# Optimization experiments

Hardware: AMD Instinct MI355X
Metric: run time of the kernel (lower is better)

## Reference

```python
import jax, jax.numpy as jnp
import numpy as np

T_STEPS = 4
LAYERS = 10
CYCLE = 10
C = 64
TAU = 1.2
V_TH = 0.5
SG_ALPHA = 4.0  # spikingjelly default surrogate.Sigmoid alpha


@jax.custom_vjp
def heaviside_sg(x):
    return (x >= 0.0).astype(x.dtype)

def _h_fwd(x):
    return heaviside_sg(x), x

def _h_bwd(x, g):
    s = jax.nn.sigmoid(SG_ALPHA * x)
    return (SG_ALPHA * s * (1.0 - s) * g,)

heaviside_sg.defvjp(_h_fwd, _h_bwd)


def lif(x_seq):
    # MultiStepLIFNode: v' = v + (x - (v - v_reset))/tau, hard reset to v_reset=0,
    # detach_reset=True -> spike in reset path is stop-gradient'ed.
    def step(v, x):
        v = v + (x - v) / TAU
        spike = heaviside_sg(v - V_TH)
        v = v * (1.0 - jax.lax.stop_gradient(spike))
        return v, spike
    _, spikes = jax.lax.scan(step, jnp.zeros_like(x_seq[0]), x_seq)
    return spikes


def conv_seq(x, w, b, dilation=1):
    # x: [T,B,Cin,L]; w: [Cout,Cin,K]; 'same' padding for odd K
    T, B, Ci, L = x.shape
    K = w.shape[-1]
    pad = (K - 1) * dilation // 2
    y = jax.lax.conv_general_dilated(
        x.reshape(T * B, Ci, L), w, (1,), [(pad, pad)],
        rhs_dilation=(dilation,), dimension_numbers=('NCH', 'OIH', 'NCH'))
    y = y + b[None, :, None]
    return y.reshape(T, B, -1, L)


def setup_inputs() -> dict:
    key = jax.random.key(0)
    ks = jax.random.split(key, 20)
    B, L = 4, 4096
    s = 0.1
    n = jax.random.normal
    inp = {
        'audio': jax.random.uniform(ks[0], (B, L), dtype=jnp.float32),
        'diffusion_step': jax.random.randint(ks[1], (B,), 0, 50),
        'W_in': n(ks[2], (C, 1, 1), jnp.float32) * s,
        'b_in': n(ks[3], (C,), jnp.float32) * s,
        'demb_w1': n(ks[4], (LAYERS, C, 1), jnp.float32) * s,
        'demb_b1': n(ks[5], (LAYERS, C), jnp.float32) * s,
        'demb_w2': n(ks[6], (LAYERS, C, C), jnp.float32) * s,
        'demb_b2': n(ks[7], (LAYERS, C), jnp.float32) * s,
        'dproj_w': n(ks[8], (LAYERS, C, C), jnp.float32) * s,
        'dproj_b': n(ks[9], (LAYERS, C), jnp.float32) * s,
        'conv_w': n(ks[10], (LAYERS, 2 * C, C, 3), jnp.float32) * 0.05,
        'conv_b': n(ks[11], (LAYERS, 2 * C), jnp.float32) * s,
        'skip_w': n(ks[12], (LAYERS, C, C, 1), jnp.float32) * s,
        'skip_b': n(ks[13], (LAYERS, C), jnp.float32) * s,
        'res_w': n(ks[14], (LAYERS, C, C, 1), jnp.float32) * s,
        'res_b': n(ks[15], (LAYERS, C), jnp.float32) * s,
        'W_out': n(ks[16], (1, C, 1), jnp.float32) * s,
        'b_out': n(ks[17], (1,), jnp.float32) * s,
    }
    return inp


def reference(audio, diffusion_step, W_in, b_in, demb_w1, demb_b1, demb_w2,
              demb_b2, dproj_w, dproj_b, conv_w, conv_b, skip_w, skip_b,
              res_w, res_b, W_out, b_out):
    B, L = audio.shape
    # Poisson encoder: spike = 1[u < x] per timestep (fixed key -> deterministic)
    u = jax.random.uniform(jax.random.key(42), (T_STEPS, B, 1, L), dtype=jnp.float32)
    spike_seq = (u < audio[None, :, None, :]).astype(jnp.float32)

    x = conv_seq(spike_seq, W_in, b_in)          # [T,B,C,L]
    x = lif(x)

    d = diffusion_step.astype(jnp.float32)[:, None]  # [B,1]
    total_skip = jnp.zeros_like(x)
    for i in range(LAYERS):
        dilation = 2 ** (i % CYCLE)
        emb = jax.nn.silu(d @ demb_w1[i].T + demb_b1[i]) @ demb_w2[i].T + demb_b2[i]  # [B,C]
        proj = emb @ dproj_w[i].T + dproj_b[i]                                        # [B,C]
        y = x + proj[None, :, :, None]
        y = conv_seq(y, conv_w[i], conv_b[i], dilation=dilation)  # [T,B,2C,L]
        y = lif(y)
        gate, filt = jnp.split(y, 2, axis=2)
        y = jax.nn.sigmoid(gate) * jnp.tanh(filt)
        total_skip = total_skip + conv_seq(y, skip_w[i], skip_b[i])
        x = x + conv_seq(y, res_w[i], res_b[i])

    total_skip = jax.nn.relu(total_skip)
    out = conv_seq(total_skip, W_out, b_out)  # [T,B,1,L]
    out = lif(out)
    return out.sum(axis=0)  # [B,1,L]
```

## Files before the change

### kernel.cpp

```cpp
#include <hip/hip_runtime.h>

#define LL 4096
#define NB 4
#define NC 64
#define NT 4
#define NLAYERS 10
#define XS 5120
#define XPAD 512

typedef float v2f __attribute__((ext_vector_type(2)));

typedef __attribute__((address_space(4))) const float cfloat;
__device__ __forceinline__ cfloat* to_constant(const float* p) {
  return (cfloat*)(unsigned long long)p;
}

__device__ __forceinline__ void threefry2x32(unsigned x0, unsigned x1,
                                             unsigned& o0, unsigned& o1) {
  const unsigned ks0 = 0u, ks1 = 42u;
  const unsigned ks2 = 0x1BD11BDAu ^ ks0 ^ ks1;
  const unsigned ks[3] = {ks0, ks1, ks2};
  const unsigned r0[4] = {13u, 15u, 26u, 6u};
  const unsigned r1[4] = {17u, 29u, 16u, 24u};
  x0 += ks0; x1 += ks1;
#pragma unroll
  for (int g = 0; g < 5; ++g) {
    const unsigned* rr = (g & 1) ? r1 : r0;
#pragma unroll
    for (int j = 0; j < 4; ++j) {
      x0 += x1;
      unsigned r = rr[j];
      x1 = (x1 << r) | (x1 >> (32u - r));
      x1 ^= x0;
    }
    x0 += ks[(g + 1) % 3];
    x1 += ks[(g + 2) % 3] + (unsigned)(g + 1);
  }
  o0 = x0; o1 = x1;
}

__device__ __forceinline__ float u01(unsigned bits) {
  return __uint_as_float((bits >> 9) | 0x3f800000u) - 1.0f;
}

__device__ __forceinline__ float lif_step(float& v, float xt) {
  v = v + (xt - v) / 1.2f;
  float s = (v >= 0.5f) ? 1.0f : 0.0f;
  v = v * (1.0f - s);
  return s;
}

__global__ void prep_kernel(const float* __restrict__ skip_w,
                            const float* __restrict__ res_w,
                            const float* __restrict__ conv_w,
                            float* __restrict__ skipT,
                            float* __restrict__ resT,
                            float* __restrict__ wT) {
  int i = blockIdx.x;
  for (int idx = threadIdx.x; idx < 4096; idx += 256) {
    int c = idx >> 6, cp = idx & 63;
    skipT[i * 4096 + cp * 64 + c] = skip_w[i * 4096 + c * 64 + cp];
    resT[i * 4096 + cp * 64 + c] = res_w[i * 4096 + c * 64 + cp];
  }
  for (int idx = threadIdx.x; idx < 16 * 64 * 3 * 8; idx += 256) {
    int col = idx & 7;
    int r = idx >> 3;
    int k = r % 3; r /= 3;
    int ci = r % 64;
    int g = r / 64;
    int co = (col < 4) ? (g * 4 + col) : (64 + g * 4 + (col - 4));
    wT[i * 24576 + idx] = conv_w[(i * 128 + co) * 192 + ci * 3 + k];
  }
}

__global__ void proj_kernel(const int* __restrict__ dstep,
                            const float* __restrict__ w1, const float* __restrict__ b1,
                            const float* __restrict__ w2, const float* __restrict__ b2,
                            const float* __restrict__ pw, const float* __restrict__ pb,
                            float* __restrict__ proj) {
  __shared__ float e1[NB][NC];
  __shared__ float e2[NB][NC];
  int i = blockIdx.x;
  int tid = threadIdx.x;
  int b = tid >> 6, c = tid & 63;
  float d = (float)dstep[b];
  float v = d * w1[i * 64 + c] + b1[i * 64 + c];
  v = v / (1.0f + expf(-v));
  e1[b][c] = v;
  __syncthreads();
  float a = b2[i * 64 + c];
  for (int cp = 0; cp < 64; ++cp) a += e1[b][cp] * w2[(i * 64 + c) * 64 + cp];
  e2[b][c] = a;
  __syncthreads();
  float p = pb[i * 64 + c];
  for (int cp = 0; cp < 64; ++cp) p += e2[b][cp] * pw[(i * 64 + c) * 64 + cp];
  proj[(i * 4 + b) * 64 + c] = p;
}

__global__ void pc_kernel(const float* __restrict__ proj,
                          const float* __restrict__ conv_w,
                          float* __restrict__ pc) {
  __shared__ float pv[64];
  int layer = blockIdx.x, b = blockIdx.y;
  int tid = threadIdx.x;
  if (tid < 64) pv[tid] = proj[(layer * 4 + b) * 64 + tid];
  __syncthreads();
  int co = tid;
  const float* w = conv_w + (layer * 128 + co) * 192;
  float s0 = 0.0f, s1 = 0.0f, s2 = 0.0f;
  for (int ci = 0; ci < 64; ++ci) {
    float p = pv[ci];
    s0 += p * w[ci * 3 + 0];
    s1 += p * w[ci * 3 + 1];
    s2 += p * w[ci * 3 + 2];
  }
  float* o = pc + ((layer * 4 + b) * 128 + co) * 3;
  o[0] = s0; o[1] = s1; o[2] = s2;
}

__global__ void padzero_kernel(float* __restrict__ x) {
  int row = blockIdx.x;
  float* base = x + (size_t)row * XS * 4;
  for (int i = threadIdx.x; i < XPAD; i += 256) {
    *(float4*)&base[i * 4] = float4{0.f, 0.f, 0.f, 0.f};
    *(float4*)&base[(XPAD + LL + i) * 4] = float4{0.f, 0.f, 0.f, 0.f};
  }
}

__global__ void encode_lif_kernel(const float* __restrict__ audio,
                                  const float* __restrict__ W_in,
                                  const float* __restrict__ b_in,
                                  float* __restrict__ x) {
  int tid = threadIdx.x;
  int lq = tid & 63, grp = tid >> 6;
  int l = blockIdx.x * 64 + lq;
  int b = blockIdx.y;
  float a = audio[b * LL + l];
  unsigned p0 = (unsigned)(b * LL + l);
  unsigned p1 = 16384u + p0;
  unsigned o00, o01, o10, o11;
  threefry2x32(p0, p0 + 32768u, o00, o01);
  threefry2x32(p1, p1 + 32768u, o10, o11);
  float sp[4];
  sp[0] = (u01(o00) < a) ? 1.0f : 0.0f;
  sp[1] = (u01(o10) < a) ? 1.0f : 0.0f;
  sp[2] = (u01(o01) < a) ? 1.0f : 0.0f;
  sp[3] = (u01(o11) < a) ? 1.0f : 0.0f;
  for (int j = 0; j < 16; ++j) {
    int c = grp * 16 + j;
    float w = W_in[c], bb = b_in[c];
    float v = 0.0f;
    float4 o;
    float* op = (float*)&o;
#pragma unroll
    for (int t = 0; t < 4; ++t) op[t] = lif_step(v, w * sp[t] + bb);
    *(float4*)&x[(size_t)((b * 64 + c) * XS + XPAD + l) * 4] = o;
  }
}

template <int DIL>
__global__ __launch_bounds__(256) void layer_conv_kernel(
    const float* __restrict__ x, const float* __restrict__ wT,
    const float* __restrict__ conv_b, const float* __restrict__ pc,
    float* __restrict__ y, int layer) {
  int tid = threadIdx.x;
  int g = blockIdx.y;
  int b = blockIdx.z;
  int l = blockIdx.x * 256 + tid;
  cfloat* cw = to_constant(wT + (size_t)(layer * 16 + g) * 1536);

  const float* px = x + (size_t)(b * 64 * XS + XPAD + l) * 4;

  float acc[8][4];
#pragma unroll
  for (int j = 0; j < 8; ++j)
#pragma unroll
    for (int t = 0; t < 4; ++t) acc[j][t] = 0.0f;

  float4 xa[3], xb[3];
  float wA[3][8], wB[3][8];

  auto loadx = [&](float4* dst) {
    dst[0] = *(const float4*)(px - (size_t)DIL * 4);
    dst[1] = *(const float4*)px;
    dst[2] = *(const float4*)(px + (size_t)DIL * 4);
    px += (size_t)XS * 4;
  };
  auto loadw = [&](int ci, float (*w)[8]) {
#pragma unroll
    for (int k = 0; k < 3; ++k)
#pragma unroll
      for (int j = 0; j < 8; ++j)
        w[k][j] = cw[(ci * 3 + k) * 8 + j];
  };
  auto compute = [&](const float (*w)[8], const float4* xv) {
#pragma unroll
    for (int k = 0; k < 3; ++k) {
      const float* xk = (const float*)&xv[k];
#pragma unroll
      for (int t = 0; t < 4; ++t) {
        float xq = xk[t];
#pragma unroll
        for (int j = 0; j < 8; ++j)
          acc[j][t] += w[k][j] * xq;
      }
    }
  };

  loadx(xa);
  loadw(0, wA);
  for (int ci = 0; ci < 64; ci += 2) {
    loadx(xb);
    loadw(ci + 1, wB);
    compute(wA, xa);
    if (ci + 2 < 64) {
      loadx(xa);
      loadw(ci + 2, wA);
    }
    compute(wB, xb);
  }

  const float SIG1 = 0.73105857863000489f;
  const float TANH1 = 0.76159415595576486f;
  bool lb = (l < DIL), rb = (l >= LL - DIL);
#pragma unroll
  for (int j = 0; j < 4; ++j) {
    int cog = g * 4 + j;
    int cof = 64 + g * 4 + j;
    const float* pg = pc + ((layer * 4 + b) * 128 + cog) * 3;
    const float* pf = pc + ((layer * 4 + b) * 128 + cof) * 3;
    float S0g = pg[0], S1g = pg[1], S2g = pg[2];
    float S0f = pf[0], S1f = pf[1], S2f = pf[2];
    float bg = conv_b[layer * 128 + cog] + S0g + S1g + S2g;
    float bf = conv_b[layer * 128 + cof] + S0f + S1f + S2f;
    bg -= (lb ? S0g : 0.0f) + (rb ? S2g : 0.0f);
    bf -= (lb ? S0f : 0.0f) + (rb ? S2f : 0.0f);
    float vg = 0.0f, vf = 0.0f;
    float4 o;
    float* op = (float*)&o;
#pragma unroll
    for (int t = 0; t < 4; ++t) {
      float av = acc[j][t];
      float fv = acc[j + 4][t];
      float sg = lif_step(vg, av + bg);
      float sf = lif_step(vf, fv + bf);
      float gv = (sg != 0.0f) ? SIG1 : 0.5f;
      float tv = (sf != 0.0f) ? TANH1 : 0.0f;
      op[t] = gv * tv;
    }
    *(float4*)&y[(size_t)((b * 64 + cog) * LL + l) * 4] = o;
  }
}

__global__ __launch_bounds__(256) void skip_res_kernel(
    const float* __restrict__ y, const float* __restrict__ skipT,
    const float* __restrict__ resT, const float* __restrict__ skip_b,
    const float* __restrict__ res_b, float* __restrict__ tskip,
    float* __restrict__ x, int layer) {
  int tid = threadIdx.x;
  int lg = tid & 31;
  int cg = tid >> 5;
  int cv = blockIdx.y;
  int b = blockIdx.z;
  int l0 = blockIdx.x * 64 + lg * 2;
  int c0 = cg * 8;

  const float* wsrc = (cv ? resT : skipT) + layer * 4096 + c0;
  const float* yb = y + (size_t)(b * 64 * LL + l0) * 4;

  v2f acc[32];
#pragma unroll
  for (int q = 0; q < 32; ++q) acc[q] = (v2f)(0.0f);

  float4 w0a = *(const float4*)&wsrc[0];
  float4 w1a = *(const float4*)&wsrc[4];
  float4 y0a = *(const float4*)yb;
  float4 y1a = *(const float4*)(yb + 4);

  for (int cp = 0; cp < 64; ++cp) {
    int cpn = (cp < 63) ? cp + 1 : 63;
    float4 w0b = *(const float4*)&wsrc[cpn * 64];
    float4 w1b = *(const float4*)&wsrc[cpn * 64 + 4];
    float4 y0b = *(const float4*)(yb + (size_t)cpn * LL * 4);
    float4 y1b = *(const float4*)(yb + (size_t)cpn * LL * 4 + 4);

    float wv[8] = {w0a.x, w0a.y, w0a.z, w0a.w, w1a.x, w1a.y, w1a.z, w1a.w};
    const v2f* yp0 = (const v2f*)&y0a;
    const v2f* yp1 = (const v2f*)&y1a;
#pragma unroll
    for (int i = 0; i < 8; ++i) {
      v2f w2;
      w2.x = wv[i]; w2.y = wv[i];
      acc[i * 4 + 0] += w2 * yp0[0];
      acc[i * 4 + 1] += w2 * yp0[1];
      acc[i * 4 + 2] += w2 * yp1[0];
      acc[i * 4 + 3] += w2 * yp1[1];
    }
    w0a = w0b; w1a = w1b; y0a = y0b; y1a = y1b;
  }

  const float* bsrc = (cv ? res_b : skip_b) + layer * 64 + c0;
#pragma unroll
  for (int i = 0; i < 8; ++i) {
    float bb = bsrc[i];
    float r[8];
#pragma unroll
    for (int q = 0; q < 4; ++q) {
      r[q * 2 + 0] = acc[i * 4 + q][0] + bb;
      r[q * 2 + 1] = acc[i * 4 + q][1] + bb;
    }
    if (cv == 0) {
      size_t idx = (size_t)((b * 64 + c0 + i) * LL + l0) * 4;
      float4 o0, o1;
      if (layer == 0) {
        o0 = float4{0.f, 0.f, 0.f, 0.f};
        o1 = o0;
      } else {
        o0 = *(const float4*)&tskip[idx];
        o1 = *(const float4*)&tskip[idx + 4];
      }
      o0.x += r[0]; o0.y += r[1]; o0.z += r[2]; o0.w += r[3];
      o1.x += r[4]; o1.y += r[5]; o1.z += r[6]; o1.w += r[7];
      *(float4*)&tskip[idx] = o0;
      *(float4*)&tskip[idx + 4] = o1;
    } else {
      size_t idx = (size_t)((b * 64 + c0 + i) * XS + XPAD + l0) * 4;
      float4 o0 = *(const float4*)&x[idx];
      float4 o1 = *(const float4*)&x[idx + 4];
      o0.x += r[0]; o0.y += r[1]; o0.z += r[2]; o0.w += r[3];
      o1.x += r[4]; o1.y += r[5]; o1.z += r[6]; o1.w += r[7];
      *(float4*)&x[idx] = o0;
      *(float4*)&x[idx + 4] = o1;
    }
  }
}

__global__ void out_kernel(const float* __restrict__ tskip,
                           const float* __restrict__ W_out,
                           const float* __restrict__ b_out,
                           float* __restrict__ out) {
  __shared__ float red[4][4][64];
  int tid = threadIdx.x;
  int lq = tid & 63, grp = tid >> 6;
  int l = blockIdx.x * 64 + lq;
  int b = blockIdx.y;
  float acc[4] = {0.0f, 0.0f, 0.0f, 0.0f};
  for (int j = 0; j < 16; ++j) {
    int c = grp * 16 + j;
    float w = W_out[c];
    float4 sv = *(const float4*)&tskip[(size_t)((b * 64 + c) * LL + l) * 4];
    acc[0] += fmaxf(sv.x, 0.0f) * w;
    acc[1] += fmaxf(sv.y, 0.0f) * w;
    acc[2] += fmaxf(sv.z, 0.0f) * w;
    acc[3] += fmaxf(sv.w, 0.0f) * w;
  }
#pragma unroll
  for (int t = 0; t < 4; ++t) red[grp][t][lq] = acc[t];
  __syncthreads();
  if (grp == 0) {
    float bo = b_out[0];
    float v = 0.0f, s = 0.0f;
#pragma unroll
    for (int t = 0; t < 4; ++t) {
      float a = red[0][t][lq] + red[1][t][lq] + red[2][t][lq] + red[3][t][lq] + bo;
      s += lif_step(v, a);
    }
    out[b * LL + l] = s;
  }
}

extern "C" void kernel_launch(void* const* d_in, const int* in_sizes, int n_in,
                              void* d_out, int out_size, void* d_ws, size_t ws_size,
                              hipStream_t stream) {
  const float* audio   = (const float*)d_in[0];
  const int*   dstep   = (const int*)d_in[1];
  const float* W_in    = (const float*)d_in[2];
  const float* b_in    = (const float*)d_in[3];
  const float* demb_w1 = (const float*)d_in[4];
  const float* demb_b1 = (const float*)d_in[5];
  const float* demb_w2 = (const float*)d_in[6];
  const float* demb_b2 = (const float*)d_in[7];
  const float* dproj_w = (const float*)d_in[8];
  const float* dproj_b = (const float*)d_in[9];
  const float* conv_w  = (const float*)d_in[10];
  const float* conv_b  = (const float*)d_in[11];
  const float* skip_w  = (const float*)d_in[12];
  const float* skip_b  = (const float*)d_in[13];
  const float* res_w   = (const float*)d_in[14];
  const float* res_b   = (const float*)d_in[15];
  const float* W_out   = (const float*)d_in[16];
  const float* b_out   = (const float*)d_in[17];
  float* out = (float*)d_out;
  float* ws = (float*)d_ws;

  float* proj  = ws;
  float* skipT = proj + 2560;
  float* resT  = skipT + 40960;
  float* pc    = resT + 40960;
  float* wT    = pc + 15360;
  float* x     = wT + 245760;
  float* y     = x + 5242880;
  float* tskip = y + 4194304;

  prep_kernel<<<10, 256, 0, stream>>>(skip_w, res_w, conv_w, skipT, resT, wT);
  proj_kernel<<<10, 256, 0, stream>>>(dstep, demb_w1, demb_b1, demb_w2, demb_b2,
                                      dproj_w, dproj_b, proj);
  pc_kernel<<<dim3(10, 4), 128, 0, stream>>>(proj, conv_w, pc);
  padzero_kernel<<<256, 256, 0, stream>>>(x);
  encode_lif_kernel<<<dim3(64, 4), 256, 0, stream>>>(audio, W_in, b_in, x);

  for (int i = 0; i < NLAYERS; ++i) {
    dim3 gc(16, 16, 4);
    switch (i) {
      case 0: layer_conv_kernel<1><<<gc, 256, 0, stream>>>(x, wT, conv_b, pc, y, i); break;
      case 1: layer_conv_kernel<2><<<gc, 256, 0, stream>>>(x, wT, conv_b, pc, y, i); break;
      case 2: layer_conv_kernel<4><<<gc, 256, 0, stream>>>(x, wT, conv_b, pc, y, i); break;
      case 3: layer_conv_kernel<8><<<gc, 256, 0, stream>>>(x, wT, conv_b, pc, y, i); break;
      case 4: layer_conv_kernel<16><<<gc, 256, 0, stream>>>(x, wT, conv_b, pc, y, i); break;
      case 5: layer_conv_kernel<32><<<gc, 256, 0, stream>>>(x, wT, conv_b, pc, y, i); break;
      case 6: layer_conv_kernel<64><<<gc, 256, 0, stream>>>(x, wT, conv_b, pc, y, i); break;
      case 7: layer_conv_kernel<128><<<gc, 256, 0, stream>>>(x, wT, conv_b, pc, y, i); break;
      case 8: layer_conv_kernel<256><<<gc, 256, 0, stream>>>(x, wT, conv_b, pc, y, i); break;
      case 9: layer_conv_kernel<512><<<gc, 256, 0, stream>>>(x, wT, conv_b, pc, y, i); break;
    }
    skip_res_kernel<<<dim3(64, 2, 4), 256, 0, stream>>>(y, skipT, resT, skip_b,
                                                        res_b, tskip, x, i);
  }
  out_kernel<<<dim3(64, 4), 256, 0, stream>>>(tskip, W_out, b_out, out);
}
```

Measured before the change: 809.1 us.

## Deepen input prefetch in layer conv and restructure skip/res GEMM with uniform weights

```diff
diff --git a/kernel.cpp b/kernel.cpp
--- a/kernel.cpp
+++ b/kernel.cpp
@@ -177,14 +177,18 @@
 #pragma unroll
     for (int t = 0; t < 4; ++t) acc[j][t] = 0.0f;
 
-  float4 xa[3], xb[3];
+  float4 P[2][3], Q[2][3];
   float wA[3][8], wB[3][8];
 
-  auto loadx = [&](float4* dst) {
-    dst[0] = *(const float4*)(px - (size_t)DIL * 4);
-    dst[1] = *(const float4*)px;
-    dst[2] = *(const float4*)(px + (size_t)DIL * 4);
-    px += (size_t)XS * 4;
+  auto loadx2 = [&](float4 (*dst)[3], int ci) {
+    const float* p = px + (size_t)ci * XS * 4;
+#pragma unroll
+    for (int j = 0; j < 2; ++j) {
+      dst[j][0] = *(const float4*)(p - (size_t)DIL * 4);
+      dst[j][1] = *(const float4*)p;
+      dst[j][2] = *(const float4*)(p + (size_t)DIL * 4);
+      p += (size_t)XS * 4;
+    }
   };
   auto loadw = [&](int ci, float (*w)[8]) {
 #pragma unroll
@@ -207,17 +211,20 @@
     }
   };
 
-  loadx(xa);
+  loadx2(P, 0);
+  loadx2(Q, 2);
   loadw(0, wA);
-  for (int ci = 0; ci < 64; ci += 2) {
-    loadx(xb);
+  for (int ci = 0; ci < 64; ci += 4) {
     loadw(ci + 1, wB);
-    compute(wA, xa);
-    if (ci + 2 < 64) {
-      loadx(xa);
-      loadw(ci + 2, wA);
-    }
-    compute(wB, xb);
+    compute(wA, P[0]);
+    loadw(ci + 2, wA);
+    compute(wB, P[1]);
+    if (ci + 4 < 64) loadx2(P, ci + 4);
+    loadw(ci + 3, wB);
+    compute(wA, Q[0]);
+    loadw((ci + 4 < 64) ? (ci + 4) : 63, wA);
+    compute(wB, Q[1]);
+    if (ci + 6 < 64) loadx2(Q, ci + 6);
   }
 
   const float SIG1 = 0.73105857863000489f;
@@ -258,79 +265,79 @@
     const float* __restrict__ res_b, float* __restrict__ tskip,
     float* __restrict__ x, int layer) {
   int tid = threadIdx.x;
-  int lg = tid & 31;
-  int cg = tid >> 5;
+  int lane = tid & 63;
+  int wid = tid >> 6;
   int cv = blockIdx.y;
   int b = blockIdx.z;
-  int l0 = blockIdx.x * 64 + lg * 2;
-  int c0 = cg * 8;
-
-  const float* wsrc = (cv ? resT : skipT) + layer * 4096 + c0;
-  const float* yb = y + (size_t)(b * 64 * LL + l0) * 4;
-
-  v2f acc[32];
-#pragma unroll
-  for (int q = 0; q < 32; ++q) acc[q] = (v2f)(0.0f);
-
-  float4 w0a = *(const float4*)&wsrc[0];
-  float4 w1a = *(const float4*)&wsrc[4];
-  float4 y0a = *(const float4*)yb;
-  float4 y1a = *(const float4*)(yb + 4);
-
-  for (int cp = 0; cp < 64; ++cp) {
-    int cpn = (cp < 63) ? cp + 1 : 63;
-    float4 w0b = *(const float4*)&wsrc[cpn * 64];
-    float4 w1b = *(const float4*)&wsrc[cpn * 64 + 4];
-    float4 y0b = *(const float4*)(yb + (size_t)cpn * LL * 4);
-    float4 y1b = *(const float4*)(yb + (size_t)cpn * LL * 4 + 4);
-
-    float wv[8] = {w0a.x, w0a.y, w0a.z, w0a.w, w1a.x, w1a.y, w1a.z, w1a.w};
-    const v2f* yp0 = (const v2f*)&y0a;
-    const v2f* yp1 = (const v2f*)&y1a;
-#pragma unroll
-    for (int i = 0; i < 8; ++i) {
-      v2f w2;
-      w2.x = wv[i]; w2.y = wv[i];
-      acc[i * 4 + 0] += w2 * yp0[0];
-      acc[i * 4 + 1] += w2 * yp0[1];
-      acc[i * 4 + 2] += w2 * yp1[0];
-      acc[i * 4 + 3] += w2 * yp1[1];
-    }
-    w0a = w0b; w1a = w1b; y0a = y0b; y1a = y1b;
+  int l = blockIdx.x * 64 + lane;
+  int c0 = wid * 16;
+
+  cfloat* cw = to_constant((cv ? resT : skipT) + layer * 4096 + c0);
+  const float* yb = y + (size_t)(b * 64 * LL + l) * 4;
+
+  float acc[16][4];
+#pragma unroll
+  for (int i = 0; i < 16; ++i)
+#pragma unroll
+    for (int t = 0; t < 4; ++t) acc[i][t] = 0.0f;
+
+  float4 P[2], Q[2];
+  float wA[16], wB[16];
+
+  auto loady2 = [&](float4* dst, int cp) {
+    dst[0] = *(const float4*)(yb + (size_t)cp * LL * 4);
+    dst[1] = *(const float4*)(yb + (size_t)(cp + 1) * LL * 4);
+  };
+  auto loadw = [&](int cp, float* w) {
+#pragma unroll
+    for (int i = 0; i < 16; ++i) w[i] = cw[cp * 64 + i];
+  };
+  auto comp = [&](const float* w, const float4& yv) {
+    const float* yt = (const float*)&yv;
+#pragma unroll
+    for (int i = 0; i < 16; ++i)
+#pragma unroll
+      for (int t = 0; t < 4; ++t)
+        acc[i][t] += w[i] * yt[t];
+  };
+
+  loady2(P, 0);
+  loady2(Q, 2);
+  loadw(0, wA);
+  for (int cp = 0; cp < 64; cp += 4) {
+    loadw(cp + 1, wB);
+    comp(wA, P[0]);
+    loadw(cp + 2, wA);
+    comp(wB, P[1]);
+    if (cp + 4 < 64) loady2(P, cp + 4);
+    loadw(cp + 3, wB);
+    comp(wA, Q[0]);
+    loadw((cp + 4 < 64) ? (cp + 4) : 63, wA);
+    comp(wB, Q[1]);
+    if (cp + 6 < 64) loady2(Q, cp + 6);
   }
 
   const float* bsrc = (cv ? res_b : skip_b) + layer * 64 + c0;
 #pragma unroll
-  for (int i = 0; i < 8; ++i) {
+  for (int i = 0; i < 16; ++i) {
     float bb = bsrc[i];
-    float r[8];
-#pragma unroll
-    for (int q = 0; q < 4; ++q) {
-      r[q * 2 + 0] = acc[i * 4 + q][0] + bb;
-      r[q * 2 + 1] = acc[i * 4 + q][1] + bb;
-    }
+    float r0 = acc[i][0] + bb, r1 = acc[i][1] + bb;
+    float r2 = acc[i][2] + bb, r3 = acc[i][3] + bb;
     if (cv == 0) {
-      size_t idx = (size_t)((b * 64 + c0 + i) * LL + l0) * 4;
-      float4 o0, o1;
+      size_t idx = (size_t)((b * 64 + c0 + i) * LL + l) * 4;
+      float4 o0;
       if (layer == 0) {
         o0 = float4{0.f, 0.f, 0.f, 0.f};
-        o1 = o0;
       } else {
         o0 = *(const float4*)&tskip[idx];
-        o1 = *(const float4*)&tskip[idx + 4];
       }
-      o0.x += r[0]; o0.y += r[1]; o0.z += r[2]; o0.w += r[3];
-      o1.x += r[4]; o1.y += r[5]; o1.z += r[6]; o1.w += r[7];
+      o0.x += r0; o0.y += r1; o0.z += r2; o0.w += r3;
       *(float4*)&tskip[idx] = o0;
-      *(float4*)&tskip[idx + 4] = o1;
     } else {
-      size_t idx = (size_t)((b * 64 + c0 + i) * XS + XPAD + l0) * 4;
+      size_t idx = (size_t)((b * 64 + c0 + i) * XS + XPAD + l) * 4;
       float4 o0 = *(const float4*)&x[idx];
-      float4 o1 = *(const float4*)&x[idx + 4];
-      o0.x += r[0]; o0.y += r[1]; o0.z += r[2]; o0.w += r[3];
-      o1.x += r[4]; o1.y += r[5]; o1.z += r[6]; o1.w += r[7];
+      o0.x += r0; o0.y += r1; o0.z += r2; o0.w += r3;
       *(float4*)&x[idx] = o0;
-      *(float4*)&x[idx + 4] = o1;
     }
   }
 }
```

Measured after the change: 1.069 ms. 1.32x slower.

## Compute two positions per thread in conv and fuse skip/res into one pass

Applied to the files above, without the earlier changes.

```diff
diff --git a/kernel.cpp b/kernel.cpp
--- a/kernel.cpp
+++ b/kernel.cpp
@@ -159,31 +159,36 @@
 }
 
 template <int DIL>
-__global__ __launch_bounds__(256) void layer_conv_kernel(
+__global__ __launch_bounds__(128, 4) void layer_conv_kernel(
     const float* __restrict__ x, const float* __restrict__ wT,
     const float* __restrict__ conv_b, const float* __restrict__ pc,
     float* __restrict__ y, int layer) {
   int tid = threadIdx.x;
   int g = blockIdx.y;
   int b = blockIdx.z;
-  int l = blockIdx.x * 256 + tid;
+  int l = blockIdx.x * 256 + tid * 2;
   cfloat* cw = to_constant(wT + (size_t)(layer * 16 + g) * 1536);
 
   const float* px = x + (size_t)(b * 64 * XS + XPAD + l) * 4;
 
-  float acc[8][4];
+  float acc[8][8];
 #pragma unroll
   for (int j = 0; j < 8; ++j)
 #pragma unroll
-    for (int t = 0; t < 4; ++t) acc[j][t] = 0.0f;
-
-  float4 xa[3], xb[3];
+    for (int q = 0; q < 8; ++q) acc[j][q] = 0.0f;
+
+  float4 xa[6], xb[6];
   float wA[3][8], wB[3][8];
 
   auto loadx = [&](float4* dst) {
-    dst[0] = *(const float4*)(px - (size_t)DIL * 4);
-    dst[1] = *(const float4*)px;
-    dst[2] = *(const float4*)(px + (size_t)DIL * 4);
+    const float* p0 = px - (size_t)DIL * 4;
+    const float* p2 = px + (size_t)DIL * 4;
+    dst[0] = *(const float4*)p0;
+    dst[1] = *(const float4*)(p0 + 4);
+    dst[2] = *(const float4*)px;
+    dst[3] = *(const float4*)(px + 4);
+    dst[4] = *(const float4*)p2;
+    dst[5] = *(const float4*)(p2 + 4);
     px += (size_t)XS * 4;
   };
   auto loadw = [&](int ci, float (*w)[8]) {
@@ -196,13 +201,16 @@
   auto compute = [&](const float (*w)[8], const float4* xv) {
 #pragma unroll
     for (int k = 0; k < 3; ++k) {
-      const float* xk = (const float*)&xv[k];
-#pragma unroll
-      for (int t = 0; t < 4; ++t) {
-        float xq = xk[t];
-#pragma unroll
-        for (int j = 0; j < 8; ++j)
-          acc[j][t] += w[k][j] * xq;
+#pragma unroll
+      for (int ll = 0; ll < 2; ++ll) {
+        const float* xk = (const float*)&xv[k * 2 + ll];
+#pragma unroll
+        for (int t = 0; t < 4; ++t) {
+          float xq = xk[t];
+#pragma unroll
+          for (int j = 0; j < 8; ++j)
+            acc[j][ll * 4 + t] += w[k][j] * xq;
+        }
       }
     }
   };
@@ -222,7 +230,9 @@
 
   const float SIG1 = 0.73105857863000489f;
   const float TANH1 = 0.76159415595576486f;
-  bool lb = (l < DIL), rb = (l >= LL - DIL);
+  bool lb[2], rb[2];
+  lb[0] = (l < DIL);     rb[0] = (l >= LL - DIL);
+  lb[1] = (l + 1 < DIL); rb[1] = (l + 1 >= LL - DIL);
 #pragma unroll
   for (int j = 0; j < 4; ++j) {
     int cog = g * 4 + j;
@@ -231,24 +241,27 @@
     const float* pf = pc + ((layer * 4 + b) * 128 + cof) * 3;
     float S0g = pg[0], S1g = pg[1], S2g = pg[2];
     float S0f = pf[0], S1f = pf[1], S2f = pf[2];
-    float bg = conv_b[layer * 128 + cog] + S0g + S1g + S2g;
-    float bf = conv_b[layer * 128 + cof] + S0f + S1f + S2f;
-    bg -= (lb ? S0g : 0.0f) + (rb ? S2g : 0.0f);
-    bf -= (lb ? S0f : 0.0f) + (rb ? S2f : 0.0f);
-    float vg = 0.0f, vf = 0.0f;
-    float4 o;
-    float* op = (float*)&o;
-#pragma unroll
-    for (int t = 0; t < 4; ++t) {
-      float av = acc[j][t];
-      float fv = acc[j + 4][t];
-      float sg = lif_step(vg, av + bg);
-      float sf = lif_step(vf, fv + bf);
-      float gv = (sg != 0.0f) ? SIG1 : 0.5f;
-      float tv = (sf != 0.0f) ? TANH1 : 0.0f;
-      op[t] = gv * tv;
-    }
-    *(float4*)&y[(size_t)((b * 64 + cog) * LL + l) * 4] = o;
+    float bg0 = conv_b[layer * 128 + cog] + S0g + S1g + S2g;
+    float bf0 = conv_b[layer * 128 + cof] + S0f + S1f + S2f;
+#pragma unroll
+    for (int ll = 0; ll < 2; ++ll) {
+      float bg = bg0 - (lb[ll] ? S0g : 0.0f) - (rb[ll] ? S2g : 0.0f);
+      float bf = bf0 - (lb[ll] ? S0f : 0.0f) - (rb[ll] ? S2f : 0.0f);
+      float vg = 0.0f, vf = 0.0f;
+      float4 o;
+      float* op = (float*)&o;
+#pragma unroll
+      for (int t = 0; t < 4; ++t) {
+        float av = acc[j][ll * 4 + t];
+        float fv = acc[j + 4][ll * 4 + t];
+        float sg = lif_step(vg, av + bg);
+        float sf = lif_step(vf, fv + bf);
+        float gv = (sg != 0.0f) ? SIG1 : 0.5f;
+        float tv = (sf != 0.0f) ? TANH1 : 0.0f;
+        op[t] = gv * tv;
+      }
+      *(float4*)&y[(size_t)((b * 64 + cog) * LL + l + ll) * 4] = o;
+    }
   }
 }
 
@@ -258,59 +271,63 @@
     const float* __restrict__ res_b, float* __restrict__ tskip,
     float* __restrict__ x, int layer) {
   int tid = threadIdx.x;
-  int lg = tid & 31;
-  int cg = tid >> 5;
-  int cv = blockIdx.y;
-  int b = blockIdx.z;
-  int l0 = blockIdx.x * 64 + lg * 2;
-  int c0 = cg * 8;
-
-  const float* wsrc = (cv ? resT : skipT) + layer * 4096 + c0;
+  int lg = tid & 15;
+  int cg = tid >> 4;
+  int b = blockIdx.y;
+  int l0 = blockIdx.x * 32 + lg * 2;
+  int c0 = cg * 4;
+
+  const float* ws_ = skipT + layer * 4096 + c0;
+  const float* wr_ = resT + layer * 4096 + c0;
   const float* yb = y + (size_t)(b * 64 * LL + l0) * 4;
 
-  v2f acc[32];
-#pragma unroll
-  for (int q = 0; q < 32; ++q) acc[q] = (v2f)(0.0f);
-
-  float4 w0a = *(const float4*)&wsrc[0];
-  float4 w1a = *(const float4*)&wsrc[4];
+  v2f as_[16], ar_[16];
+#pragma unroll
+  for (int q = 0; q < 16; ++q) {
+    as_[q] = (v2f)(0.0f);
+    ar_[q] = (v2f)(0.0f);
+  }
+
+  float4 wsa = *(const float4*)&ws_[0];
+  float4 wra = *(const float4*)&wr_[0];
   float4 y0a = *(const float4*)yb;
   float4 y1a = *(const float4*)(yb + 4);
 
   for (int cp = 0; cp < 64; ++cp) {
     int cpn = (cp < 63) ? cp + 1 : 63;
-    float4 w0b = *(const float4*)&wsrc[cpn * 64];
-    float4 w1b = *(const float4*)&wsrc[cpn * 64 + 4];
+    float4 wsb = *(const float4*)&ws_[cpn * 64];
+    float4 wrb = *(const float4*)&wr_[cpn * 64];
     float4 y0b = *(const float4*)(yb + (size_t)cpn * LL * 4);
     float4 y1b = *(const float4*)(yb + (size_t)cpn * LL * 4 + 4);
 
-    float wv[8] = {w0a.x, w0a.y, w0a.z, w0a.w, w1a.x, w1a.y, w1a.z, w1a.w};
+    float wsv[4] = {wsa.x, wsa.y, wsa.z, wsa.w};
+    float wrv[4] = {wra.x, wra.y, wra.z, wra.w};
     const v2f* yp0 = (const v2f*)&y0a;
     const v2f* yp1 = (const v2f*)&y1a;
 #pragma unroll
-    for (int i = 0; i < 8; ++i) {
-      v2f w2;
-      w2.x = wv[i]; w2.y = wv[i];
-      acc[i * 4 + 0] += w2 * yp0[0];
-      acc[i * 4 + 1] += w2 * yp0[1];
-      acc[i * 4 + 2] += w2 * yp1[0];
-      acc[i * 4 + 3] += w2 * yp1[1];
-    }
-    w0a = w0b; w1a = w1b; y0a = y0b; y1a = y1b;
-  }
-
-  const float* bsrc = (cv ? res_b : skip_b) + layer * 64 + c0;
-#pragma unroll
-  for (int i = 0; i < 8; ++i) {
-    float bb = bsrc[i];
-    float r[8];
-#pragma unroll
-    for (int q = 0; q < 4; ++q) {
-      r[q * 2 + 0] = acc[i * 4 + q][0] + bb;
-      r[q * 2 + 1] = acc[i * 4 + q][1] + bb;
-    }
-    if (cv == 0) {
-      size_t idx = (size_t)((b * 64 + c0 + i) * LL + l0) * 4;
+    for (int i = 0; i < 4; ++i) {
+      v2f w2s, w2r;
+      w2s.x = wsv[i]; w2s.y = wsv[i];
+      w2r.x = wrv[i]; w2r.y = wrv[i];
+      as_[i * 4 + 0] += w2s * yp0[0];
+      as_[i * 4 + 1] += w2s * yp0[1];
+      as_[i * 4 + 2] += w2s * yp1[0];
+      as_[i * 4 + 3] += w2s * yp1[1];
+      ar_[i * 4 + 0] += w2r * yp0[0];
+      ar_[i * 4 + 1] += w2r * yp0[1];
+      ar_[i * 4 + 2] += w2r * yp1[0];
+      ar_[i * 4 + 3] += w2r * yp1[1];
+    }
+    wsa = wsb; wra = wrb; y0a = y0b; y1a = y1b;
+  }
+
+#pragma unroll
+  for (int i = 0; i < 4; ++i) {
+    int c = c0 + i;
+    float sb = skip_b[layer * 64 + c];
+    float rb = res_b[layer * 64 + c];
+    {
+      size_t idx = (size_t)((b * 64 + c) * LL + l0) * 4;
       float4 o0, o1;
       if (layer == 0) {
         o0 = float4{0.f, 0.f, 0.f, 0.f};
@@ -319,16 +336,29 @@
         o0 = *(const float4*)&tskip[idx];
         o1 = *(const float4*)&tskip[idx + 4];
       }
-      o0.x += r[0]; o0.y += r[1]; o0.z += r[2]; o0.w += r[3];
-      o1.x += r[4]; o1.y += r[5]; o1.z += r[6]; o1.w += r[7];
+      o0.x += as_[i * 4 + 0][0] + sb;
+      o0.y += as_[i * 4 + 0][1] + sb;
+      o0.z += as_[i * 4 + 1][0] + sb;
+      o0.w += as_[i * 4 + 1][1] + sb;
+      o1.x += as_[i * 4 + 2][0] + sb;
+      o1.y += as_[i * 4 + 2][1] + sb;
+      o1.z += as_[i * 4 + 3][0] + sb;
+      o1.w += as_[i * 4 + 3][1] + sb;
       *(float4*)&tskip[idx] = o0;
       *(float4*)&tskip[idx + 4] = o1;
-    } else {
-      size_t idx = (size_t)((b * 64 + c0 + i) * XS + XPAD + l0) * 4;
+    }
+    {
+      size_t idx = (size_t)((b * 64 + c) * XS + XPAD + l0) * 4;
       float4 o0 = *(const float4*)&x[idx];
       float4 o1 = *(const float4*)&x[idx + 4];
-      o0.x += r[0]; o0.y += r[1]; o0.z += r[2]; o0.w += r[3];
-      o1.x += r[4]; o1.y += r[5]; o1.z += r[6]; o1.w += r[7];
+      o0.x += ar_[i * 4 + 0][0] + rb;
+      o0.y += ar_[i * 4 + 0][1] + rb;
+      o0.z += ar_[i * 4 + 1][0] + rb;
+      o0.w += ar_[i * 4 + 1][1] + rb;
+      o1.x += ar_[i * 4 + 2][0] + rb;
+      o1.y += ar_[i * 4 + 2][1] + rb;
+      o1.z += ar_[i * 4 + 3][0] + rb;
+      o1.w += ar_[i * 4 + 3][1] + rb;
       *(float4*)&x[idx] = o0;
       *(float4*)&x[idx + 4] = o1;
     }
@@ -412,19 +442,19 @@
   for (int i = 0; i < NLAYERS; ++i) {
     dim3 gc(16, 16, 4);
     switch (i) {
-      case 0: layer_conv_kernel<1><<<gc, 256, 0, stream>>>(x, wT, conv_b, pc, y, i); break;
-      case 1: layer_conv_kernel<2><<<gc, 256, 0, stream>>>(x, wT, conv_b, pc, y, i); break;
-      case 2: layer_conv_kernel<4><<<gc, 256, 0, stream>>>(x, wT, conv_b, pc, y, i); break;
-      case 3: layer_conv_kernel<8><<<gc, 256, 0, stream>>>(x, wT, conv_b, pc, y, i); break;
-      case 4: layer_conv_kernel<16><<<gc, 256, 0, stream>>>(x, wT, conv_b, pc, y, i); break;
-      case 5: layer_conv_kernel<32><<<gc, 256, 0, stream>>>(x, wT, conv_b, pc, y, i); break;
-      case 6: layer_conv_kernel<64><<<gc, 256, 0, stream>>>(x, wT, conv_b, pc, y, i); break;
-      case 7: layer_conv_kernel<128><<<gc, 256, 0, stream>>>(x, wT, conv_b, pc, y, i); break;
-      case 8: layer_conv_kernel<256><<<gc, 256, 0, stream>>>(x, wT, conv_b, pc, y, i); break;
-      case 9: layer_conv_kernel<512><<<gc, 256, 0, stream>>>(x, wT, conv_b, pc, y, i); break;
-    }
-    skip_res_kernel<<<dim3(64, 2, 4), 256, 0, stream>>>(y, skipT, resT, skip_b,
-                                                        res_b, tskip, x, i);
+      case 0: layer_conv_kernel<1><<<gc, 128, 0, stream>>>(x, wT, conv_b, pc, y, i); break;
+      case 1: layer_conv_kernel<2><<<gc, 128, 0, stream>>>(x, wT, conv_b, pc, y, i); break;
+      case 2: layer_conv_kernel<4><<<gc, 128, 0, stream>>>(x, wT, conv_b, pc, y, i); break;
+      case 3: layer_conv_kernel<8><<<gc, 128, 0, stream>>>(x, wT, conv_b, pc, y, i); break;
+      case 4: layer_conv_kernel<16><<<gc, 128, 0, stream>>>(x, wT, conv_b, pc, y, i); break;
+      case 5: layer_conv_kernel<32><<<gc, 128, 0, stream>>>(x, wT, conv_b, pc, y, i); break;
+      case 6: layer_conv_kernel<64><<<gc, 128, 0, stream>>>(x, wT, conv_b, pc, y, i); break;
+      case 7: layer_conv_kernel<128><<<gc, 128, 0, stream>>>(x, wT, conv_b, pc, y, i); break;
+      case 8: layer_conv_kernel<256><<<gc, 128, 0, stream>>>(x, wT, conv_b, pc, y, i); break;
+      case 9: layer_conv_kernel<512><<<gc, 128, 0, stream>>>(x, wT, conv_b, pc, y, i); break;
+    }
+    skip_res_kernel<<<dim3(128, 4), 256, 0, stream>>>(y, skipT, resT, skip_b,
+                                                      res_b, tskip, x, i);
   }
   out_kernel<<<dim3(64, 4), 256, 0, stream>>>(tskip, W_out, b_out, out);
 }
```

Measured after the change: 932.7 us. 1.15x slower.
